# Optimization experiments

Measured on AMD Instinct MI355X. Metric: run time of the kernel, lower is better.

The kernel has to match this reference:

```python
import jax, jax.numpy as jnp
from jax import lax
import numpy as np

K_TOP = 100
NMS_THRESH = 0.5
SUBJECT_CATEGORY_ID = 0


def box_cxcywh_to_xyxy(b):
    cx, cy, w, h = b[..., 0], b[..., 1], b[..., 2], b[..., 3]
    return jnp.stack([cx - 0.5 * w, cy - 0.5 * h, cx + 0.5 * w, cy + 0.5 * h], axis=-1)


def _pairwise_iou(boxes):
    # boxes: [K,4] xyxy; uses the +1 pixel convention from the original numpy NMS
    x1, y1, x2, y2 = boxes[:, 0], boxes[:, 1], boxes[:, 2], boxes[:, 3]
    area = (x2 - x1 + 1.0) * (y2 - y1 + 1.0)
    xx1 = jnp.maximum(x1[:, None], x1[None, :])
    yy1 = jnp.maximum(y1[:, None], y1[None, :])
    xx2 = jnp.minimum(x2[:, None], x2[None, :])
    yy2 = jnp.minimum(y2[:, None], y2[None, :])
    w = jnp.maximum(0.0, xx2 - xx1 + 1.0)
    h = jnp.maximum(0.0, yy2 - yy1 + 1.0)
    inter = w * h
    union = area[:, None] + area[None, :] - inter
    return inter / union


def _nms_keep(sub_boxes, obj_boxes, obj_labels, hoi_scores):
    # Greedy grouped pairwise NMS for one image.
    # Grouping key degenerates to object label (subject cat and verb-row are constant).
    K = sub_boxes.shape[0]
    max_scores = hoi_scores.max(axis=-1)
    order = jnp.argsort(-max_scores)
    ovr = _pairwise_iou(sub_boxes) * _pairwise_iou(obj_boxes)  # [K,K]
    same_group = obj_labels[:, None] == obj_labels[None, :]
    ovr = jnp.where(same_group, ovr, 0.0)
    ovr_s = ovr[order][:, order]
    upper = jnp.triu(jnp.ones((K, K), dtype=bool), k=1)
    sup_mat = (ovr_s > NMS_THRESH) & upper  # suppression only of later (lower-score) items

    def body(i, st):
        suppressed, keep = st
        ki = jnp.logical_not(suppressed[i])
        keep = keep.at[i].set(ki)
        suppressed = suppressed | (ki & sup_mat[i])
        return suppressed, keep

    _, keep_sorted = lax.fori_loop(0, K, body, (jnp.zeros(K, bool), jnp.zeros(K, bool)))
    return jnp.zeros(K, bool).at[order].set(keep_sorted)


def setup_inputs() -> dict:
    key = jax.random.key(0)
    k1, k2, k3, k4, k5, k6 = jax.random.split(key, 6)
    B, Q, C, V = 256, 300, 81, 117
    return {
        "pred_obj_logits": jax.random.normal(k1, (B, Q, C), dtype=jnp.float32),
        "pred_verb_logits": jax.random.normal(k2, (B, Q, V), dtype=jnp.float32),
        "pred_sub_boxes": jax.random.uniform(k3, (B, Q, 4), dtype=jnp.float32),
        "pred_obj_boxes": jax.random.uniform(k4, (B, Q, 4), dtype=jnp.float32),
        "correct_mat": (jax.random.uniform(k5, (V, C), dtype=jnp.float32) > 0.3).astype(jnp.float32),
        "target_sizes": jax.random.randint(k6, (B, 2), 200, 640, dtype=jnp.int32),
    }


def reference(pred_obj_logits, pred_verb_logits, pred_sub_boxes, pred_obj_boxes, correct_mat, target_sizes):
    B, Q, C = pred_obj_logits.shape
    V = pred_verb_logits.shape[-1]

    obj_prob = jax.nn.softmax(pred_obj_logits, axis=-1)       # [B,Q,C]  (no_obj=False)
    verb_scores = jax.nn.sigmoid(pred_verb_logits)            # [B,Q,V]

    topk_values, topk_indexes = lax.top_k(obj_prob.reshape(B, Q * C), K_TOP)  # [B,100]
    topk_boxes = topk_indexes // C
    obj_labels = topk_indexes % C

    vs = jnp.take_along_axis(verb_scores, topk_boxes[..., None], axis=1)      # [B,100,V]
    ob = jnp.take_along_axis(pred_obj_boxes, topk_boxes[..., None], axis=1)   # [B,100,4]
    sb = jnp.take_along_axis(pred_sub_boxes, topk_boxes[..., None], axis=1)

    img_h = target_sizes[:, 0].astype(jnp.float32)
    img_w = target_sizes[:, 1].astype(jnp.float32)
    scale_fct = jnp.stack([img_w, img_h, img_w, img_h], axis=1)  # [B,4]
    sub_boxes = box_cxcywh_to_xyxy(sb) * scale_fct[:, None, :]
    obj_boxes = box_cxcywh_to_xyxy(ob) * scale_fct[:, None, :]

    hoi_scores = vs * topk_values[..., None]                    # [B,100,V]
    # masks[b,k,v] = correct_mat[v, obj_labels[b,k]]
    masks = correct_mat.T[obj_labels]                           # [B,100,V]
    hoi_scores = hoi_scores * masks

    keep = jax.vmap(_nms_keep)(sub_boxes, obj_boxes, obj_labels, hoi_scores)  # [B,100] bool
    final_scores = hoi_scores * keep[..., None].astype(hoi_scores.dtype)

    return final_scores, topk_values, obj_labels, sub_boxes, obj_boxes, keep
```

## Files before the change

kernel.cpp:

```cpp
#include <hip/hip_runtime.h>
#include <cmath>

#pragma clang fp contract(off)

#define NT 1024
constexpr int B_ = 256, Q_ = 300, C_ = 81, V_ = 117, K_ = 100;
constexpr int QC_ = Q_ * C_;
constexpr int KV_ = K_ * V_;
constexpr int CAP = 1024;
constexpr int CMN = V_ * C_;

using u32 = unsigned int;
using u64 = unsigned long long;
using u16 = unsigned short;
using u8  = unsigned char;

constexpr u32 PCUT_BITS = 0x3C000000u;
constexpr int BIN0 = 480;
constexpr int NB   = 64;

constexpr int OFF_CM   = 0;
constexpr int OFF_HIST = 37920;
constexpr int OFF_RMAX = OFF_HIST + 8192;
constexpr int OFF_RINV = OFF_RMAX + 1240;
constexpr int OFF_BSUB = OFF_RINV + 1240;
constexpr int OFF_BOBJ = OFF_BSUB + 1600;
constexpr int OFF_SUPR = OFF_BOBJ + 1600;
constexpr int OFF_SELV = OFF_SUPR + 1600;
constexpr int OFF_SELI = OFF_SELV + 400;
constexpr int OFF_MAXB = OFF_SELI + 400;
constexpr int OFF_ORD  = OFF_MAXB + 400;
constexpr int OFF_LAB  = OFF_ORD + 104;
constexpr int OFF_MISC = OFF_LAB + 104;
constexpr int SMEM_SZ  = OFF_MISC + 48;
static_assert(SMEM_SZ <= 65536, "LDS overflow");
static_assert((OFF_BSUB & 15) == 0 && (OFF_BOBJ & 15) == 0, "b128 align");
static_assert(OFF_HIST >= OFF_CM + CMN * 4, "cm/hist overlap");
static_assert((OFF_HIST & 7) == 0, "cand u64 align");

__device__ __forceinline__ void bar_lds() {
    asm volatile("s_waitcnt lgkmcnt(0)\n\ts_barrier" ::: "memory");
}

__device__ __forceinline__ int RM(int r) { return r + (r >> 5); }

__device__ __forceinline__ u64 shfl_xor_u64(u64 v, int mask) {
    u32 lo = (u32)v, hi = (u32)(v >> 32);
    lo = (u32)__shfl_xor((int)lo, mask, 64);
    hi = (u32)__shfl_xor((int)hi, mask, 64);
    return ((u64)hi << 32) | lo;
}

template <int CTRL>
__device__ __forceinline__ int dpp_i(int x) {
    return __builtin_amdgcn_update_dpp(0, x, CTRL, 0xF, 0xF, true);
}
__device__ __forceinline__ float bfly16(float x){ return __int_as_float(__builtin_amdgcn_ds_swizzle(__float_as_int(x), 0x401F)); }
__device__ __forceinline__ float bfly8 (float x){ return __int_as_float(dpp_i<0x128>(__float_as_int(x))); }
__device__ __forceinline__ float bfly4 (float x){ return __int_as_float(__builtin_amdgcn_ds_swizzle(__float_as_int(x), 0x101F)); }
__device__ __forceinline__ float bfly2 (float x){ return __int_as_float(dpp_i<0x4E>(__float_as_int(x))); }
__device__ __forceinline__ float bfly1 (float x){ return __int_as_float(dpp_i<0xB1>(__float_as_int(x))); }
__device__ __forceinline__ int ibfly4(int x){ return __builtin_amdgcn_ds_swizzle(x, 0x101F); }
__device__ __forceinline__ int ibfly2(int x){ return dpp_i<0x4E>(x); }
__device__ __forceinline__ int ibfly1(int x){ return dpp_i<0xB1>(x); }

__device__ __forceinline__ float iou4(float4 a, float4 b, float areaSum) {
    float xx1 = fmaxf(a.x, b.x);
    float yy1 = fmaxf(a.y, b.y);
    float xx2 = fminf(a.z, b.z);
    float yy2 = fminf(a.w, b.w);
    float w = fmaxf(0.f, xx2 - xx1 + 1.f);
    float h = fmaxf(0.f, yy2 - yy1 + 1.f);
    float inter = w * h;
    return inter / (areaSum - inter);
}

__global__ __launch_bounds__(NT, 4) void hoi_kernel(
    const float* __restrict__ obj_logits,
    const float* __restrict__ verb_logits,
    const float* __restrict__ sub_boxes_in,
    const float* __restrict__ obj_boxes_in,
    const float* __restrict__ cm,
    const int*   __restrict__ tsizes,
    float* __restrict__ out)
{
    const int b = blockIdx.x;
    const int tid = threadIdx.x;

    __shared__ __align__(16) u8 smem[SMEM_SZ];
    float* cml     = (float*)(smem + OFF_CM);
    u32*   hist    = (u32*)(smem + OFF_HIST);
    u64*   cand    = (u64*)(smem + OFF_HIST);
    float* asub    = (float*)(smem + OFF_HIST);
    float* aobj    = (float*)(smem + OFF_HIST + 512);
    float* rowmax  = (float*)(smem + OFF_RMAX);
    float* rinv    = (float*)(smem + OFF_RINV);
    float (*bsub)[4]   = (float(*)[4])(smem + OFF_BSUB);
    float (*bobj)[4]   = (float(*)[4])(smem + OFF_BOBJ);
    u32   (*supcol)[4] = (u32(*)[4])(smem + OFF_SUPR);
    float* sel_val = (float*)(smem + OFF_SELV);
    u32*   sel_idx = (u32*)(smem + OFF_SELI);
    u32*   maxbits = (u32*)(smem + OFF_MAXB);
    u8*    order8  = (u8*)(smem + OFF_ORD);
    u8*    lab8    = (u8*)(smem + OFF_LAB);
    u32*   skeep     = (u32*)(smem + OFF_MISC);
    u32*   keep_bits = (u32*)(smem + OFF_MISC + 16);
    u32*   s_cnt     = (u32*)(smem + OFF_MISC + 32);
    int*   sT        = (int*)(smem + OFF_MISC + 36);
    u64*   wred    = (u64*)(smem + OFF_BOBJ);
    u64*   s_prev  = (u64*)(smem + OFF_SUPR);

    const float* lg = obj_logits + (size_t)b * QC_;

    float* o0 = out;
    float* o1 = out + (size_t)B_ * KV_;
    float* o2 = o1 + (size_t)B_ * K_;
    float* o3 = o2 + (size_t)B_ * K_;
    float* o4 = o3 + (size_t)B_ * K_ * 4;
    float* o5 = o4 + (size_t)B_ * K_ * 4;

    if (tid < NB) hist[tid] = 0;
    if (tid == 0) *s_cnt = 0;
    {
        constexpr int CM4 = CMN / 4;
        for (int i = tid; i < CM4; i += NT)
            ((float4*)cml)[i] = ((const float4*)cm)[i];
        if (tid == 0) cml[CMN - 1] = cm[CMN - 1];
    }
    bar_lds();

    const int g = tid >> 5, l = tid & 31;
    const bool have2 = (l < C_ - 64);
    u32 cmask = 0;
    {
        float v0[10], v1[10], v2[10];
        #pragma unroll
        for (int s = 0; s < 10; ++s) {
            int r = g + 32 * s;
            const float* row = lg + (size_t)((r < Q_ ? r : Q_ - 1) * C_);
            v0[s] = row[l];
            v1[s] = row[l + 32];
            v2[s] = have2 ? row[l + 64] : -INFINITY;
        }
        float m[10];
        #pragma unroll
        for (int s = 0; s < 10; ++s) m[s] = fmaxf(fmaxf(v0[s], v1[s]), v2[s]);
        #pragma unroll
        for (int s = 0; s < 10; ++s) m[s] = fmaxf(m[s], bfly16(m[s]));
        #pragma unroll
        for (int s = 0; s < 10; ++s) m[s] = fmaxf(m[s], bfly8(m[s]));
        #pragma unroll
        for (int s = 0; s < 10; ++s) m[s] = fmaxf(m[s], bfly4(m[s]));
        #pragma unroll
        for (int s = 0; s < 10; ++s) m[s] = fmaxf(m[s], bfly2(m[s]));
        #pragma unroll
        for (int s = 0; s < 10; ++s) m[s] = fmaxf(m[s], bfly1(m[s]));
        float e0[10], e1[10], e2[10], sm[10];
        #pragma unroll
        for (int s = 0; s < 10; ++s) {
            e0[s] = expf(v0[s] - m[s]);
            e1[s] = expf(v1[s] - m[s]);
            e2[s] = have2 ? expf(v2[s] - m[s]) : 0.f;
            sm[s] = e0[s] + e1[s] + e2[s];
        }
        #pragma unroll
        for (int s = 0; s < 10; ++s) sm[s] += bfly16(sm[s]);
        #pragma unroll
        for (int s = 0; s < 10; ++s) sm[s] += bfly8(sm[s]);
        #pragma unroll
        for (int s = 0; s < 10; ++s) sm[s] += bfly4(sm[s]);
        #pragma unroll
        for (int s = 0; s < 10; ++s) sm[s] += bfly2(sm[s]);
        #pragma unroll
        for (int s = 0; s < 10; ++s) sm[s] += bfly1(sm[s]);
        #pragma unroll
        for (int s = 0; s < 10; ++s) {
            int r = g + 32 * s;
            if (r < Q_) {
                float ri = 1.f / sm[s];
                float p0 = e0[s] * ri, p1 = e1[s] * ri;
                u32 x0 = __float_as_uint(p0), x1 = __float_as_uint(p1);
                if (x0 >= PCUT_BITS) {
                    atomicAdd(&hist[(x0 >> 21) - BIN0], 1u);
                    cmask |= 1u << (3 * s);
                }
                if (x1 >= PCUT_BITS) {
                    atomicAdd(&hist[(x1 >> 21) - BIN0], 1u);
                    cmask |= 1u << (3 * s + 1);
                }
                if (have2) {
                    float p2 = e2[s] * ri;
                    u32 x2 = __float_as_uint(p2);
                    if (x2 >= PCUT_BITS) {
                        atomicAdd(&hist[(x2 >> 21) - BIN0], 1u);
                        cmask |= 1u << (3 * s + 2);
                    }
                }
                if (l == 0) { rowmax[RM(r)] = m[s]; rinv[RM(r)] = ri; }
            }
        }
    }
    bar_lds();

    if (tid < 64) {
        u32 suf = hist[tid];
        #pragma unroll
        for (int off = 1; off < 64; off <<= 1) {
            u32 o = (u32)__shfl_down((int)suf, off, 64);
            suf += (tid + off < 64) ? o : 0;
        }
        u32 nxt = (u32)__shfl_down((int)suf, 1, 64);
        if (tid == 63) nxt = 0;
        if (suf >= (u32)K_ && nxt < (u32)K_) *sT = BIN0 + tid;
    }
    bar_lds();
    const int T = *sT;

    u32 mk = cmask;
    while (mk) {
        int bpos = (int)__builtin_ctz(mk);
        mk &= mk - 1;
        int s = (bpos * 171) >> 9;
        int c = bpos - 3 * s;
        int r = g + 32 * s;
        int col = l + 32 * c;
        int i = r * C_ + col;
        float p = expf(lg[i] - rowmax[RM(r)]) * rinv[RM(r)];
        u32 xb = __float_as_uint(p);
        if ((int)(xb >> 21) >= T) {
            u32 pos = atomicAdd(s_cnt, 1u);
            if (pos < (u32)CAP)
                cand[pos] = ((u64)xb << 32) | (u32)(~i);
        }
    }
    bar_lds();
    const int ncand = (int)*s_cnt;

    if (ncand <= CAP) {
        if (tid < ncand) {
            u64 mykey = cand[tid];
            int rank = 0;
            int f = 0;
            for (; f + 4 <= ncand; f += 4) {
                u64 k0 = cand[f], k1 = cand[f + 1];
                u64 k2 = cand[f + 2], k3 = cand[f + 3];
                rank += (k0 > mykey) ? 1 : 0;
                rank += (k1 > mykey) ? 1 : 0;
                rank += (k2 > mykey) ? 1 : 0;
                rank += (k3 > mykey) ? 1 : 0;
            }
            for (; f < ncand; ++f) rank += (cand[f] > mykey) ? 1 : 0;
            if (rank < K_) {
                sel_val[rank] = __uint_as_float((u32)(mykey >> 32));
                sel_idx[rank] = ~(u32)mykey;
            }
        }
    } else {
        if (tid == 0) *s_prev = ~0ull;
        __syncthreads();
        for (int r = 0; r < K_; r++) {
            u64 prev = *s_prev;
            u64 local = 0;
            for (int i = tid; i < QC_; i += NT) {
                int q = i / C_;
                float p = expf(lg[i] - rowmax[RM(q)]) * rinv[RM(q)];
                u64 key = ((u64)__float_as_uint(p) << 32) | (u32)(~i);
                if (key < prev && key > local) local = key;
            }
            for (int off = 32; off > 0; off >>= 1) {
                u64 o = shfl_xor_u64(local, off);
                if (o > local) local = o;
            }
            if ((tid & 63) == 0) wred[tid >> 6] = local;
            __syncthreads();
            if (tid == 0) {
                u64 m = wred[0];
                for (int wv = 1; wv < 16; wv++) if (wred[wv] > m) m = wred[wv];
                *s_prev = m;
                u32 idx = ~(u32)m;
                if (idx >= (u32)QC_) idx = 0;
                sel_val[r] = __uint_as_float((u32)(m >> 32));
                sel_idx[r] = idx;
            }
            __syncthreads();
        }
    }
    bar_lds();

    if (tid < 800) {
        int c = tid >> 3, j = tid & 7;
        u32 idx = sel_idx[c];
        int q = (int)idx / C_, lab = (int)idx - q * C_;
        const float* vrow = verb_logits + ((size_t)b * Q_ + q) * V_;
        float* orow = o0 + (size_t)b * KV_ + c * V_;
        float sv = sel_val[c];
        float m = 0.f;
        #pragma unroll
        for (int k = 0; k < 15; ++k) {
            int v = j + 8 * k;
            if (v < V_) {
                float x = vrow[v];
                float cv = cml[v * C_ + lab];
                float hv = (1.f / (1.f + expf(-x))) * sv * cv;
                orow[v] = hv;
                m = fmaxf(m, hv);
            }
        }
        m = fmaxf(m, bfly4(m));
        m = fmaxf(m, bfly2(m));
        m = fmaxf(m, bfly1(m));
        if (j == 0) { maxbits[c] = __float_as_uint(m); lab8[c] = (u8)lab; }
    } else if (tid < 900) {
        int t = tid - 800;
        int idx = (int)sel_idx[t];
        int q = idx / C_;
        float iw = (float)tsizes[b * 2 + 1];
        float ih = (float)tsizes[b * 2 + 0];
        float4 sb = ((const float4*)sub_boxes_in)[(size_t)b * Q_ + q];
        float x1 = (sb.x - 0.5f * sb.z) * iw, y1 = (sb.y - 0.5f * sb.w) * ih;
        float x2 = (sb.x + 0.5f * sb.z) * iw, y2 = (sb.y + 0.5f * sb.w) * ih;
        bsub[t][0] = x1; bsub[t][1] = y1; bsub[t][2] = x2; bsub[t][3] = y2;
        asub[t] = (x2 - x1 + 1.f) * (y2 - y1 + 1.f);
        supcol[t][0] = 0; supcol[t][1] = 0; supcol[t][2] = 0; supcol[t][3] = 0;
    } else if (tid < 1000) {
        int t = tid - 900;
        int idx = (int)sel_idx[t];
        int q = idx / C_;
        float iw = (float)tsizes[b * 2 + 1];
        float ih = (float)tsizes[b * 2 + 0];
        float4 ob = ((const float4*)obj_boxes_in)[(size_t)b * Q_ + q];
        float x1 = (ob.x - 0.5f * ob.z) * iw, y1 = (ob.y - 0.5f * ob.w) * ih;
        float x2 = (ob.x + 0.5f * ob.z) * iw, y2 = (ob.y + 0.5f * ob.w) * ih;
        bobj[t][0] = x1; bobj[t][1] = y1; bobj[t][2] = x2; bobj[t][3] = y2;
        aobj[t] = (x2 - x1 + 1.f) * (y2 - y1 + 1.f);
    } else if (tid < 1004) {
        keep_bits[tid - 1000] = 0;
    }
    bar_lds();

    if (tid < 800) {
        int r = tid >> 3, j = tid & 7;
        u64 kr = ((u64)maxbits[r] << 32) | (u32)(~r);
        int rank = 0;
        for (int k = 0; k < 13; k++) {
            int jj = j * 13 + k;
            if (jj < K_) {
                u64 kj = ((u64)maxbits[jj] << 32) | (u32)(~jj);
                rank += (kj > kr) ? 1 : 0;
            }
        }
        rank += ibfly4(rank);
        rank += ibfly2(rank);
        rank += ibfly1(rank);
        if (j == 0) order8[rank] = (u8)r;
    }
    bar_lds();

    if (tid < K_) {
        o1[(size_t)b * K_ + tid] = sel_val[tid];
        o2[(size_t)b * K_ + tid] = (float)(sel_idx[tid] % (u32)C_);
    }
    if (tid >= 128 && tid < 128 + K_ * 4) {
        int t = tid - 128;
        int r = t >> 2, k = t & 3;
        o3[((size_t)b * K_) * 4 + t] = bsub[r][k];
        o4[((size_t)b * K_) * 4 + t] = bobj[r][k];
    }

    for (int e = tid; e < K_ * K_; e += NT) {
        int i = e / K_, j = e - i * K_;
        if (j > i) {
            int ri = order8[i], rj = order8[j];
            u32 li = lab8[ri], lj = lab8[rj];
            if (li == lj) {
                float4 s_i = *(const float4*)bsub[ri];
                float4 s_j = *(const float4*)bsub[rj];
                float4 b_i = *(const float4*)bobj[ri];
                float4 b_j = *(const float4*)bobj[rj];
                float o = iou4(s_i, s_j, asub[ri] + asub[rj]) *
                          iou4(b_i, b_j, aobj[ri] + aobj[rj]);
                if (o > 0.5f)
                    atomicOr(&supcol[j][i >> 5], 1u << (i & 31));
            }
        }
    }
    bar_lds();

    if (tid < 64) {
        u32 cA[4], cB[4];
        #pragma unroll
        for (int w = 0; w < 4; ++w) cA[w] = supcol[tid][w];
        #pragma unroll
        for (int w = 0; w < 4; ++w) cB[w] = (tid < K_ - 64) ? supcol[tid + 64][w] : 0u;
        bool sA = false, sB = false;
        u32 km[4] = {0, 0, 0, 0};
        #pragma unroll
        for (int i = 0; i < 64; ++i) {
            u64 bal = __ballot(sA);
            if (!((bal >> i) & 1)) {
                km[i >> 5] |= 1u << (i & 31);
                sA = sA || ((cA[i >> 5] >> (i & 31)) & 1u);
                sB = sB || ((cB[i >> 5] >> (i & 31)) & 1u);
            }
        }
        #pragma unroll
        for (int i = 64; i < K_; ++i) {
            u64 bal = __ballot(sB);
            if (!((bal >> (i - 64)) & 1)) {
                km[i >> 5] |= 1u << (i & 31);
                sA = sA || ((cA[i >> 5] >> (i & 31)) & 1u);
                sB = sB || ((cB[i >> 5] >> (i & 31)) & 1u);
            }
        }
        if (tid == 0) { skeep[0] = km[0]; skeep[1] = km[1]; skeep[2] = km[2]; skeep[3] = km[3]; }
    }
    bar_lds();
    if (tid < K_) {
        if ((skeep[tid >> 5] >> (tid & 31)) & 1u) {
            int r = order8[tid];
            atomicOr(&keep_bits[r >> 5], 1u << (r & 31));
        }
    }
    __syncthreads();

    for (int f = tid; f < KV_; f += NT) {
        int r = f / V_;
        if (!((keep_bits[r >> 5] >> (r & 31)) & 1u))
            o0[(size_t)b * KV_ + f] = 0.f;
    }
    if (tid < K_) {
        bool kp = (keep_bits[tid >> 5] >> (tid & 31)) & 1u;
        o5[(size_t)b * K_ + tid] = kp ? 1.f : 0.f;
    }
}

extern "C" void kernel_launch(void* const* d_in, const int* in_sizes, int n_in,
                              void* d_out, int out_size, void* d_ws, size_t ws_size,
                              hipStream_t stream) {
    const float* obj_logits  = (const float*)d_in[0];
    const float* verb_logits = (const float*)d_in[1];
    const float* sub_boxes   = (const float*)d_in[2];
    const float* obj_boxes   = (const float*)d_in[3];
    const float* cm          = (const float*)d_in[4];
    const int*   ts          = (const int*)d_in[5];
    hipLaunchKernelGGL(hoi_kernel, dim3(B_), dim3(NT), 0, stream,
                       obj_logits, verb_logits, sub_boxes, obj_boxes, cm, ts,
                       (float*)d_out);
}
```

Measured before the change: 129.7 us.

## Replicate histogram bins and defer correct_mat LDS staging past top-k selection

The histogram is replicated 8 ways per bin, indexed by thread lane, to reduce LDS atomic contention. The scan then sums the replicas with two vector loads per bin. The correct_mat copy into LDS is moved from kernel start to after the candidate ranking: global loads are issued into registers before ranking and written to LDS afterwards, so their latency overlaps the selection work. This raises register pressure during ranking and relies on the cm region not overlapping the cand/hist buffers.

```diff
diff --git a/kernel.cpp b/kernel.cpp
--- a/kernel.cpp
+++ b/kernel.cpp
@@ -18,6 +18,7 @@
 constexpr u32 PCUT_BITS = 0x3C000000u;
 constexpr int BIN0 = 480;
 constexpr int NB   = 64;
+constexpr int HREP = 8;
 
 constexpr int OFF_CM   = 0;
 constexpr int OFF_HIST = 37920;
@@ -36,7 +37,7 @@
 static_assert(SMEM_SZ <= 65536, "LDS overflow");
 static_assert((OFF_BSUB & 15) == 0 && (OFF_BOBJ & 15) == 0, "b128 align");
 static_assert(OFF_HIST >= OFF_CM + CMN * 4, "cm/hist overlap");
-static_assert((OFF_HIST & 7) == 0, "cand u64 align");
+static_assert((OFF_HIST & 15) == 0, "cand/hist align");
 
 __device__ __forceinline__ void bar_lds() {
     asm volatile("s_waitcnt lgkmcnt(0)\n\ts_barrier" ::: "memory");
@@ -119,18 +120,13 @@
     float* o4 = o3 + (size_t)B_ * K_ * 4;
     float* o5 = o4 + (size_t)B_ * K_ * 4;
 
-    if (tid < NB) hist[tid] = 0;
+    if (tid < NB * HREP) hist[tid] = 0;
     if (tid == 0) *s_cnt = 0;
-    {
-        constexpr int CM4 = CMN / 4;
-        for (int i = tid; i < CM4; i += NT)
-            ((float4*)cml)[i] = ((const float4*)cm)[i];
-        if (tid == 0) cml[CMN - 1] = cm[CMN - 1];
-    }
     bar_lds();
 
     const int g = tid >> 5, l = tid & 31;
     const bool have2 = (l < C_ - 64);
+    const int hsub = tid & (HREP - 1);
     u32 cmask = 0;
     {
         float v0[10], v1[10], v2[10];
@@ -181,18 +177,18 @@
                 float p0 = e0[s] * ri, p1 = e1[s] * ri;
                 u32 x0 = __float_as_uint(p0), x1 = __float_as_uint(p1);
                 if (x0 >= PCUT_BITS) {
-                    atomicAdd(&hist[(x0 >> 21) - BIN0], 1u);
+                    atomicAdd(&hist[(((x0 >> 21) - BIN0) << 3) + hsub], 1u);
                     cmask |= 1u << (3 * s);
                 }
                 if (x1 >= PCUT_BITS) {
-                    atomicAdd(&hist[(x1 >> 21) - BIN0], 1u);
+                    atomicAdd(&hist[(((x1 >> 21) - BIN0) << 3) + hsub], 1u);
                     cmask |= 1u << (3 * s + 1);
                 }
                 if (have2) {
                     float p2 = e2[s] * ri;
                     u32 x2 = __float_as_uint(p2);
                     if (x2 >= PCUT_BITS) {
-                        atomicAdd(&hist[(x2 >> 21) - BIN0], 1u);
+                        atomicAdd(&hist[(((x2 >> 21) - BIN0) << 3) + hsub], 1u);
                         cmask |= 1u << (3 * s + 2);
                     }
                 }
@@ -203,7 +199,9 @@
     bar_lds();
 
     if (tid < 64) {
-        u32 suf = hist[tid];
+        uint4 ha = ((const uint4*)hist)[tid * 2];
+        uint4 hb = ((const uint4*)hist)[tid * 2 + 1];
+        u32 suf = ha.x + ha.y + ha.z + ha.w + hb.x + hb.y + hb.z + hb.w;
         #pragma unroll
         for (int off = 1; off < 64; off <<= 1) {
             u32 o = (u32)__shfl_down((int)suf, off, 64);
@@ -236,6 +234,14 @@
     bar_lds();
     const int ncand = (int)*s_cnt;
 
+    constexpr int CM4 = CMN / 4;
+    const float4* cmg4 = (const float4*)cm;
+    float4 cc0 = cmg4[tid];
+    float4 cc1 = cmg4[tid + NT];
+    float4 cc2 = (tid < CM4 - 2 * NT) ? cmg4[tid + 2 * NT]
+                                      : make_float4(0.f, 0.f, 0.f, 0.f);
+    float ctail = (tid == 0) ? cm[CMN - 1] : 0.f;
+
     if (ncand <= CAP) {
         if (tid < ncand) {
             u64 mykey = cand[tid];
@@ -285,6 +291,11 @@
             __syncthreads();
         }
     }
+
+    ((float4*)cml)[tid] = cc0;
+    ((float4*)cml)[tid + NT] = cc1;
+    if (tid < CM4 - 2 * NT) ((float4*)cml)[tid + 2 * NT] = cc2;
+    if (tid == 0) cml[CMN - 1] = ctail;
     bar_lds();
 
     if (tid < 800) {
```

After: 127.8 us. Within noise of the previous version (-1.4%).
